# Optimization experiments

Measured on AMD Instinct MI355X. Metric: run time of the kernel, lower is better.

The kernel has to match this reference:

```python
import jax, jax.numpy as jnp
import numpy as np

# static sizes
B, N_PER, D, H, L, DFF, IN_DIM = 32, 1024, 128, 4, 3, 2048, 64
N = B * N_PER
HD = D // H
EPS = 1e-5


def setup_inputs() -> dict:
    key = jax.random.key(0)
    ks = jax.random.split(key, 16)
    s = 0.02
    rn = lambda k, shp: jax.random.normal(k, shp, jnp.float32) * s
    return {
        "x": jax.random.normal(ks[0], (N, IN_DIM), jnp.float32),
        # uniform graph sizes -> static max_nodes; sorted graph ids
        "batch": jnp.repeat(jnp.arange(B, dtype=jnp.int32), N_PER),
        "W_in": rn(ks[1], (D, IN_DIM)),
        "b_in": rn(ks[2], (D,)),
        "Wqkv": rn(ks[3], (L, 3 * D, D)),
        "bqkv": rn(ks[4], (L, 3 * D)),
        "Wo": rn(ks[5], (L, D, D)),
        "bo": rn(ks[6], (L, D)),
        "W1": rn(ks[7], (L, DFF, D)),
        "b1": rn(ks[8], (L, DFF)),
        "W2": rn(ks[9], (L, D, DFF)),
        "b2": rn(ks[10], (L, D)),
        "ln1_g": jnp.ones((L, D), jnp.float32),
        "ln1_b": jnp.zeros((L, D), jnp.float32),
        "ln2_g": jnp.ones((L, D), jnp.float32),
        "ln2_b": jnp.zeros((L, D), jnp.float32),
    }


def _ln(x, g, b):
    m = x.mean(-1, keepdims=True)
    v = jnp.mean((x - m) ** 2, axis=-1, keepdims=True)
    return (x - m) / jnp.sqrt(v + EPS) * g + b


def _mha(h, Wqkv, bqkv, Wo, bo):
    # h: [B, S, D]
    qkv = h @ Wqkv.T + bqkv                      # [B, S, 3D]
    q, k, v = jnp.split(qkv, 3, axis=-1)
    q = q.reshape(B, -1, H, HD)
    k = k.reshape(B, -1, H, HD)
    v = v.reshape(B, -1, H, HD)
    att = jnp.einsum("bqhd,bkhd->bhqk", q, k) / np.sqrt(HD).astype(np.float32)
    p = jax.nn.softmax(att, axis=-1)
    o = jnp.einsum("bhqk,bkhd->bqhd", p, v).reshape(B, -1, D)
    return o @ Wo.T + bo


def reference(x, batch, W_in, b_in, Wqkv, bqkv, Wo, bo, W1, b1, W2, b2,
              ln1_g, ln1_b, ln2_g, ln2_b):
    # fused ragged -> padded: project all nodes once, scatter by (graph, pos)
    h = x @ W_in.T + b_in                        # [N, D]
    starts = jnp.searchsorted(batch, jnp.arange(B, dtype=batch.dtype))
    pos = jnp.arange(N, dtype=batch.dtype) - starts[batch]
    padded = jnp.zeros((B, N_PER, D), h.dtype).at[batch, pos].set(h)

    out = padded
    for l in range(L):  # post-LN TransformerEncoderLayer, dropout=eval
        a = _mha(out, Wqkv[l], bqkv[l], Wo[l], bo[l])
        out = _ln(out + a, ln1_g[l], ln1_b[l])
        f = jax.nn.relu(out @ W1[l].T + b1[l]) @ W2[l].T + b2[l]
        out = _ln(out + f, ln2_g[l], ln2_b[l])

    # mask derived from projected inputs, exactly as the original
    mask = (padded.sum(axis=2) != 0).astype(out.dtype)  # [B, S]
    return (out * mask[:, :, None]).sum(axis=1) / mask.sum(axis=1, keepdims=True)
```

## Files before the change

kernel.cpp:

```cpp
#include <hip/hip_runtime.h>
#include <hip/hip_bf16.h>
#include <stdint.h>

#define BB    32
#define NPER  1024
#define NTOT  32768
#define DD    128
#define HH    4
#define HD    32
#define LL    3
#define DFF   2048
#define INDIM 64
#define QKSCALE 0.17677669529663687f

typedef unsigned short u16;
typedef short bf16x8 __attribute__((ext_vector_type(8)));
typedef float f32x4 __attribute__((ext_vector_type(4)));

#define AS_GLOBAL(p) ((const __attribute__((address_space(1))) void*)(p))
#define AS_LDS(p)    ((__attribute__((address_space(3))) void*)(p))

__device__ __forceinline__ float bf2f(u16 v){
  unsigned u = ((unsigned)v) << 16; float f; __builtin_memcpy(&f, &u, 4); return f;
}
__device__ __forceinline__ u16 f2bf(float f){
  unsigned u; __builtin_memcpy(&u, &f, 4);
  unsigned lsb = (u >> 16) & 1u;
  u += 0x7fffu + lsb;
  return (u16)(u >> 16);
}

constexpr size_t OFF_FLAG   = 0;
constexpr size_t OFF_STARTS = 256;
constexpr size_t OFF_BIN    = 1024;
constexpr size_t OFF_BQKV   = OFF_BIN   + 128*4;
constexpr size_t OFF_BO     = OFF_BQKV  + 1152*4;
constexpr size_t OFF_B1     = OFF_BO    + 384*4;
constexpr size_t OFF_B2     = OFF_B1    + 6144*4;
constexpr size_t OFF_LN1G   = OFF_B2    + 384*4;
constexpr size_t OFF_LN1B   = OFF_LN1G  + 384*4;
constexpr size_t OFF_LN2G   = OFF_LN1B  + 384*4;
constexpr size_t OFF_LN2B   = OFF_LN2G  + 384*4;
constexpr size_t OFF_XB     = 40960;
constexpr size_t OFF_WINB   = OFF_XB    + (size_t)2097152*2;
constexpr size_t OFF_WQKVB  = OFF_WINB  + (size_t)8192*2;
constexpr size_t OFF_WOB    = OFF_WQKVB + (size_t)147456*2;
constexpr size_t OFF_W1B    = OFF_WOB   + (size_t)49152*2;
constexpr size_t OFF_W2B    = OFF_W1B   + (size_t)786432*2;
constexpr size_t OFF_CUR    = OFF_W2B   + (size_t)786432*2;
constexpr size_t OFF_TMP    = OFF_CUR   + (size_t)4194304*4;
constexpr size_t OFF_CURB   = OFF_TMP   + (size_t)4194304*4;
constexpr size_t OFF_QKVB   = OFF_CURB  + (size_t)4194304*2;
constexpr size_t OFF_ATTNOB = OFF_QKVB  + (size_t)12582912*2;
constexpr size_t OFF_ACTB   = OFF_ATTNOB+ (size_t)4194304*2;
constexpr size_t OFF_MASK   = OFF_ACTB  + (size_t)16777216*2;
constexpr size_t OFF_VT     = OFF_MASK  + (size_t)NTOT*4;
constexpr size_t OFF_RED    = OFF_VT    + (size_t)4096*1024*2;
constexpr size_t OFF_CNT    = OFF_RED   + (size_t)32*8*128*4;

__device__ __forceinline__ int plaus(unsigned bits){
  if ((bits << 1) == 0u) return 1;
  unsigned e = (bits >> 23) & 0xFFu;
  return (e >= 100u && e <= 140u) ? 1 : 0;
}
__global__ void detect_kernel(const unsigned* __restrict__ x, int* __restrict__ flag){
  __shared__ int red[256];
  int t = threadIdx.x, c = 0;
  for (int i = t; i < 2048; i += 256){
    unsigned w = x[i];
    c += (plaus(w << 16) & plaus(w & 0xFFFF0000u));
  }
  red[t] = c; __syncthreads();
  for (int s = 128; s > 0; s >>= 1){ if (t < s) red[t] += red[t+s]; __syncthreads(); }
  if (t == 0) *flag = (red[0] >= 1229) ? 1 : 0;
}

__global__ void starts_kernel(const int* __restrict__ batch, int* __restrict__ starts){
  int b = threadIdx.x;
  if (b < BB){
    int lo = 0, hi = NTOT;
    while (lo < hi){ int mid = (lo + hi) >> 1; if (batch[mid] < b) lo = mid + 1; else hi = mid; }
    starts[b] = lo;
  }
}

struct ConvSeg { const void* src; void* dst; int n; int tobf; };
struct ConvArgs { ConvSeg s[15]; };

__global__ __launch_bounds__(256) void convall_kernel(ConvArgs a, const int* __restrict__ flag){
  const int isb = *flag;
  const int blk = blockIdx.x;
  int seg = -1, base = 0, lb = 0;
  #pragma unroll
  for (int i = 0; i < 15; ++i){
    int nb = (a.s[i].n + 1023) >> 10;
    if (seg < 0){
      if (blk < base + nb){ seg = i; lb = blk - base; }
      base += nb;
    }
  }
  const ConvSeg sg = a.s[seg];
  const int idx = lb*1024 + threadIdx.x*4;
  if (idx >= sg.n) return;
  if (sg.tobf){
    u16* dst = (u16*)sg.dst + idx;
    if (isb){
      *(uint2*)dst = *(const uint2*)((const u16*)sg.src + idx);
    } else {
      const float* s4 = (const float*)sg.src + idx;
      dst[0] = f2bf(s4[0]); dst[1] = f2bf(s4[1]);
      dst[2] = f2bf(s4[2]); dst[3] = f2bf(s4[3]);
    }
  } else {
    float* dst = (float*)sg.dst + idx;
    if (isb){
      const u16* s4 = (const u16*)sg.src + idx;
      dst[0] = bf2f(s4[0]); dst[1] = bf2f(s4[1]);
      dst[2] = bf2f(s4[2]); dst[3] = bf2f(s4[3]);
    } else {
      *(float4*)dst = *(const float4*)((const float*)sg.src + idx);
    }
  }
}

__global__ __launch_bounds__(256) void gemm_bf16(
    const u16* __restrict__ A, int lda,
    const u16* __restrict__ W, int ldw,
    const float* __restrict__ bias,
    float* __restrict__ Cf, u16* __restrict__ Cb,
    int N, int K, int flags)
{
  __shared__ __align__(16) u16 At[64][32];
  __shared__ __align__(16) u16 Wt[64][32];
  const int t = threadIdx.x;
  const int m0 = blockIdx.x * 64, n0 = blockIdx.y * 64;
  const int wave = t >> 6, lane = t & 63;
  const int quad = lane >> 4, l16 = lane & 15;
  const int lr = t >> 2, lc = (t & 3) * 8;

  f32x4 acc[4];
  #pragma unroll
  for (int i = 0; i < 4; ++i){ acc[i][0]=0.f; acc[i][1]=0.f; acc[i][2]=0.f; acc[i][3]=0.f; }

  const u16* Arow = A + (size_t)(m0 + lr) * lda + lc;
  const u16* Wrow = W + (size_t)(n0 + lr) * ldw + lc;

  for (int k0 = 0; k0 < K; k0 += 32){
    uint4 av = *(const uint4*)(Arow + k0);
    uint4 wv = *(const uint4*)(Wrow + k0);
    __syncthreads();
    *(uint4*)&At[lr][lc] = av;
    *(uint4*)&Wt[lr][lc] = wv;
    __syncthreads();
    bf16x8 af = *(const bf16x8*)&At[wave*16 + l16][quad*8];
    #pragma unroll
    for (int nt = 0; nt < 4; ++nt){
      bf16x8 wf = *(const bf16x8*)&Wt[nt*16 + l16][quad*8];
      acc[nt] = __builtin_amdgcn_mfma_f32_16x16x32_bf16(af, wf, acc[nt], 0, 0, 0);
    }
  }
  const int row = m0 + wave*16 + quad*4;
  #pragma unroll
  for (int nt = 0; nt < 4; ++nt){
    const int col = n0 + nt*16 + l16;
    const float bv = bias ? bias[col] : 0.f;
    #pragma unroll
    for (int r = 0; r < 4; ++r){
      size_t idx = (size_t)(row + r) * N + col;
      float v = acc[nt][r] + bv;
      if (flags & 1) v = fmaxf(v, 0.f);
      if (Cf) Cf[idx] = v;
      if (Cb) Cb[idx] = f2bf(v);
    }
  }
}

__global__ __launch_bounds__(128) void scatter_kernel(
    const float* __restrict__ hlin, const int* __restrict__ batch,
    const int* __restrict__ starts, float* __restrict__ cur,
    u16* __restrict__ curb, float* __restrict__ mask)
{
  int i = blockIdx.x, t = threadIdx.x;
  int g = batch[i];
  int p = i - starts[g];
  float v = hlin[(size_t)i*DD + t];
  float s = v;
  #pragma unroll
  for (int off = 32; off; off >>= 1) s += __shfl_xor(s, off);
  __shared__ float sh[2];
  if ((t & 63) == 0) sh[t >> 6] = s;
  __syncthreads();
  float rowsum = sh[0] + sh[1];
  if ((unsigned)p < (unsigned)NPER && (unsigned)g < (unsigned)BB){
    size_t j = (size_t)g*NPER + p;
    cur[j*DD + t]  = v;
    curb[j*DD + t] = f2bf(v);
    if (t == 0) mask[j] = (rowsum != 0.f) ? 1.f : 0.f;
  }
}

__global__ __launch_bounds__(256) void fattn_kernel(
    const u16* __restrict__ qkvb,
    const u16* __restrict__ vt,
    u16* __restrict__ attnob)
{
  __shared__ __align__(16) u16 Klds[2][2048];
  __shared__ __align__(16) u16 Vl[2][2048];
  __shared__ __align__(16) u16 Pl[4][16*72];

  const int t = threadIdx.x;
  const int wave = t >> 6, lane = t & 63;
  const int quad = lane >> 4, l16 = lane & 15;
  const int q0 = blockIdx.x * 64;
  const int h = blockIdx.y, b = blockIdx.z;
  const size_t qkvbase = (size_t)b * NPER * 384;
  const u16* Kg = qkvb + qkvbase + 128 + h*HD;
  const u16* Vg = vt + (size_t)((b*HH + h)*HD) * NPER;

  bf16x8 qf;
  {
    const u16* qp = qkvb + qkvbase + (size_t)(q0 + wave*16 + l16)*384 + h*HD + quad*8;
    uint4 qv = *(const uint4*)qp;
    u16 raw[8]; __builtin_memcpy(raw, &qv, 16);
    #pragma unroll
    for (int j = 0; j < 8; ++j) qf[j] = (short)f2bf(bf2f(raw[j]) * QKSCALE);
  }

  const int vcv = wave*2 + (lane >> 5), vd = lane & 31;
  auto stage = [&](int buf, int kt){
    __builtin_amdgcn_global_load_lds(
        AS_GLOBAL(Kg + (size_t)(kt*64 + lane)*384 + wave*8),
        AS_LDS(&Klds[buf][wave*64*8]), 16, 0, 0);
    __builtin_amdgcn_global_load_lds(
        AS_GLOBAL(Vg + (size_t)vd*NPER + kt*64 + vcv*8),
        AS_LDS(&Vl[buf][wave*64*8]), 16, 0, 0);
  };

  float lsum = 0.f;
  f32x4 o0 = {0.f,0.f,0.f,0.f}, o1 = {0.f,0.f,0.f,0.f};
  u16* Pw = &Pl[wave][0];

  stage(0, 0);
  asm volatile("s_waitcnt vmcnt(0)" ::: "memory");
  __syncthreads();

  for (int kt = 0; kt < 16; ++kt){
    const int buf = kt & 1;
    if (kt + 1 < 16) stage(buf ^ 1, kt + 1);

    f32x4 sfr[4];
    #pragma unroll
    for (int nt = 0; nt < 4; ++nt){
      bf16x8 kf = *(const bf16x8*)&Klds[buf][(quad*64 + nt*16 + l16)*8];
      f32x4 z = {0.f,0.f,0.f,0.f};
      sfr[nt] = __builtin_amdgcn_mfma_f32_16x16x32_bf16(kf, qf, z, 0, 0, 0);
    }

    float ps = 0.f;
    #pragma unroll
    for (int nt = 0; nt < 4; ++nt){
      float e0 = __expf(sfr[nt][0]), e1 = __expf(sfr[nt][1]);
      float e2 = __expf(sfr[nt][2]), e3 = __expf(sfr[nt][3]);
      ps += (e0 + e1) + (e2 + e3);
      uint2 w;
      w.x = (unsigned)f2bf(e0) | ((unsigned)f2bf(e1) << 16);
      w.y = (unsigned)f2bf(e2) | ((unsigned)f2bf(e3) << 16);
      *(uint2*)&Pw[l16*72 + nt*16 + quad*4] = w;
    }
    ps += __shfl_xor(ps, 16);
    ps += __shfl_xor(ps, 32);
    lsum += ps;
    asm volatile("s_waitcnt lgkmcnt(0)" ::: "memory");

    #pragma unroll
    for (int kk = 0; kk < 2; ++kk){
      bf16x8 pf = *(const bf16x8*)&Pw[l16*72 + kk*32 + quad*8];
      bf16x8 v0 = *(const bf16x8*)&Vl[buf][((kk*4 + quad)*32 + l16)*8];
      bf16x8 v1 = *(const bf16x8*)&Vl[buf][((kk*4 + quad)*32 + 16 + l16)*8];
      o0 = __builtin_amdgcn_mfma_f32_16x16x32_bf16(pf, v0, o0, 0, 0, 0);
      o1 = __builtin_amdgcn_mfma_f32_16x16x32_bf16(pf, v1, o1, 0, 0, 0);
    }

    if (kt + 1 < 16){
      asm volatile("s_waitcnt vmcnt(0)" ::: "memory");
      __syncthreads();
    }
  }

  #pragma unroll
  for (int r = 0; r < 4; ++r){
    float inv = 1.f / __shfl(lsum, quad*4 + r);
    int row = q0 + wave*16 + quad*4 + r;
    size_t base = (size_t)(b*NPER + row)*DD + h*HD;
    attnob[base + l16]      = f2bf(o0[r] * inv);
    attnob[base + 16 + l16] = f2bf(o1[r] * inv);
  }
}

__device__ __forceinline__ void epilogue_ln64(
    const f32x4 O[8], int m0, int wave, int quad, int l16,
    const float* __restrict__ bias, const float* __restrict__ g,
    const float* __restrict__ beta, float* __restrict__ cur,
    u16* __restrict__ curb)
{
  #pragma unroll
  for (int rr = 0; rr < 4; ++rr){
    int row = m0 + wave*16 + quad*4 + rr;
    float vs[8], sum = 0.f;
    #pragma unroll
    for (int nt = 0; nt < 8; ++nt){
      int col = nt*16 + l16;
      float v = O[nt][rr] + bias[col] + cur[(size_t)row*DD + col];
      vs[nt] = v; sum += v;
    }
    sum += __shfl_xor(sum, 1); sum += __shfl_xor(sum, 2);
    sum += __shfl_xor(sum, 4); sum += __shfl_xor(sum, 8);
    float mean = sum * (1.f/DD);
    float sq = 0.f;
    #pragma unroll
    for (int nt = 0; nt < 8; ++nt){ float d = vs[nt] - mean; sq += d*d; }
    sq += __shfl_xor(sq, 1); sq += __shfl_xor(sq, 2);
    sq += __shfl_xor(sq, 4); sq += __shfl_xor(sq, 8);
    float rs = rsqrtf(sq * (1.f/DD) + 1e-5f);
    #pragma unroll
    for (int nt = 0; nt < 8; ++nt){
      int col = nt*16 + l16;
      float o = (vs[nt] - mean)*rs*g[col] + beta[col];
      cur[(size_t)row*DD + col]  = o;
      curb[(size_t)row*DD + col] = f2bf(o);
    }
  }
}

__global__ __launch_bounds__(256) void wgemm_kernel(
    const u16* __restrict__ A,
    const u16* __restrict__ Wbase,
    const float* __restrict__ biasb,
    int mode,
    u16* __restrict__ outb, int opitch,
    u16* __restrict__ vtout,
    float* __restrict__ cur, u16* __restrict__ curb,
    const float* __restrict__ g, const float* __restrict__ beta)
{
  __shared__ __align__(16) u16 Wl[16384];
  const int t = threadIdx.x, wave = t >> 6, lane = t & 63;
  const int quad = lane >> 4, l16 = lane & 15;
  const int m0 = blockIdx.x * 64, nb = blockIdx.y;
  const u16* Wsl = Wbase + (size_t)nb * 16384;
  const float* bias = biasb + nb * 128;

  #pragma unroll
  for (int j = 0; j < 8; ++j){
    int s = t + 256*j;
    int r = s >> 4, cx = (s & 15) ^ (r & 15);
    *(uint4*)&Wl[s*8] = *(const uint4*)(Wsl + (size_t)r*128 + cx*8);
  }
  bf16x8 af[4];
  #pragma unroll
  for (int kk = 0; kk < 4; ++kk)
    af[kk] = *(const bf16x8*)(A + (size_t)(m0 + wave*16 + l16)*128 + kk*32 + quad*8);
  __syncthreads();

  f32x4 O[8];
  #pragma unroll
  for (int nt = 0; nt < 8; ++nt){ O[nt][0]=0.f; O[nt][1]=0.f; O[nt][2]=0.f; O[nt][3]=0.f; }

  #pragma unroll
  for (int nt = 0; nt < 8; ++nt){
    int row = nt*16 + l16;
    bf16x8 wf[4];
    #pragma unroll
    for (int kk = 0; kk < 4; ++kk)
      wf[kk] = *(const bf16x8*)&Wl[(row*16 + ((kk*4 + quad) ^ l16))*8];
    #pragma unroll
    for (int kk = 0; kk < 4; ++kk)
      O[nt] = __builtin_amdgcn_mfma_f32_16x16x32_bf16(af[kk], wf[kk], O[nt], 0, 0, 0);
  }

  if (mode == 0){
    if (nb == 2 && vtout){
      int rowb = m0 + wave*16 + quad*4;
      int bg = rowb >> 10, s = rowb & 1023;
      #pragma unroll
      for (int nt = 0; nt < 8; ++nt){
        int col = nt*16 + l16;
        int hh = col >> 5, d = col & 31;
        float v0 = O[nt][0] + bias[col], v1 = O[nt][1] + bias[col];
        float v2 = O[nt][2] + bias[col], v3 = O[nt][3] + bias[col];
        uint2 w;
        w.x = (unsigned)f2bf(v0) | ((unsigned)f2bf(v1) << 16);
        w.y = (unsigned)f2bf(v2) | ((unsigned)f2bf(v3) << 16);
        *(uint2*)(vtout + (size_t)((bg*HH + hh)*HD + d)*NPER + s) = w;
      }
    } else {
      #pragma unroll
      for (int rr = 0; rr < 4; ++rr){
        int row = m0 + wave*16 + quad*4 + rr;
        #pragma unroll
        for (int nt = 0; nt < 8; ++nt){
          int col = nt*16 + l16;
          outb[(size_t)row*opitch + nb*128 + col] = f2bf(O[nt][rr] + bias[col]);
        }
      }
    }
  } else {
    epilogue_ln64(O, m0, wave, quad, l16, bias, g, beta, cur, curb);
  }
}

__global__ __launch_bounds__(256, 2) void ffn_kernel(
    const u16* __restrict__ Ag,
    const u16* __restrict__ W1g,
    const u16* __restrict__ W2g,
    const float* __restrict__ b1,
    const float* __restrict__ b2,
    const float* __restrict__ g, const float* __restrict__ beta,
    float* __restrict__ cur, u16* __restrict__ curb)
{
  __shared__ __align__(16) u16 W1l[2][8192];
  __shared__ __align__(16) u16 W2l[2][8192];
  __shared__ __align__(16) u16 Pl[4][16*72];

  const int t = threadIdx.x, wave = t >> 6, lane = t & 63;
  const int quad = lane >> 4, l16 = lane & 15;
  const int m0 = blockIdx.x * 64;
  u16* Pw = &Pl[wave][0];

  auto stage = [&](int buf, int dffc){
    #pragma unroll
    for (int i = 0; i < 4; ++i){
      const int s0 = wave*256 + i*64;
      const int s  = s0 + lane;
      { int r = s >> 4, cx = (s & 15) ^ (r & 15);
        __builtin_amdgcn_global_load_lds(
            AS_GLOBAL(W1g + (size_t)(dffc + r)*128 + cx*8),
            AS_LDS(&W1l[buf][s0*8]), 16, 0, 0); }
      { int r = s >> 3, cx = (s & 7) ^ (r & 7);
        __builtin_amdgcn_global_load_lds(
            AS_GLOBAL(W2g + (size_t)r*DFF + dffc + cx*8),
            AS_LDS(&W2l[buf][s0*8]), 16, 0, 0); }
    }
  };

  bf16x8 af[4];
  #pragma unroll
  for (int kk = 0; kk < 4; ++kk)
    af[kk] = *(const bf16x8*)(Ag + (size_t)(m0 + wave*16 + l16)*128 + kk*32 + quad*8);

  f32x4 O[8];
  #pragma unroll
  for (int nt = 0; nt < 8; ++nt){ O[nt][0]=0.f; O[nt][1]=0.f; O[nt][2]=0.f; O[nt][3]=0.f; }

  stage(0, 0);
  asm volatile("s_waitcnt vmcnt(0)" ::: "memory");
  __syncthreads();

  for (int c = 0; c < 32; ++c){
    const int buf = c & 1;
    if (c + 1 < 32) stage(buf ^ 1, (c + 1)*64);

    #pragma unroll
    for (int nt = 0; nt < 4; ++nt){
      int row = nt*16 + l16;
      bf16x8 wf[4];
      #pragma unroll
      for (int kk = 0; kk < 4; ++kk)
        wf[kk] = *(const bf16x8*)&W1l[buf][(row*16 + ((kk*4 + quad) ^ l16))*8];
      float b1v = b1[c*64 + row];
      f32x4 s = {0.f,0.f,0.f,0.f};
      #pragma unroll
      for (int kk = 0; kk < 4; ++kk)
        s = __builtin_amdgcn_mfma_f32_16x16x32_bf16(af[kk], wf[kk], s, 0, 0, 0);
      #pragma unroll
      for (int rr = 0; rr < 4; ++rr)
        Pw[(quad*4 + rr)*72 + nt*16 + l16] = f2bf(fmaxf(s[rr] + b1v, 0.f));
    }
    asm volatile("s_waitcnt lgkmcnt(0)" ::: "memory");

    bf16x8 pf[2];
    #pragma unroll
    for (int kk = 0; kk < 2; ++kk)
      pf[kk] = *(const bf16x8*)&Pw[l16*72 + kk*32 + quad*8];
    #pragma unroll
    for (int nt = 0; nt < 8; ++nt){
      int row = nt*16 + l16;
      bf16x8 wf[2];
      #pragma unroll
      for (int kk = 0; kk < 2; ++kk)
        wf[kk] = *(const bf16x8*)&W2l[buf][(row*8 + ((kk*4 + quad) ^ (l16 & 7)))*8];
      #pragma unroll
      for (int kk = 0; kk < 2; ++kk)
        O[nt] = __builtin_amdgcn_mfma_f32_16x16x32_bf16(pf[kk], wf[kk], O[nt], 0, 0, 0);
    }

    if (c + 1 < 32){
      asm volatile("s_waitcnt vmcnt(0)" ::: "memory");
      __syncthreads();
    }
  }

  epilogue_ln64(O, m0, wave, quad, l16, b2, g, beta, cur, curb);
}

__global__ __launch_bounds__(128) void reduce1_kernel(
    const float* __restrict__ cur, const float* __restrict__ mask,
    float* __restrict__ partial, float* __restrict__ cnt)
{
  int b = blockIdx.x, c = blockIdx.y, t = threadIdx.x;
  float acc = 0.f, cn = 0.f;
  for (int s = c*128; s < c*128 + 128; ++s){
    float mk = mask[b*NPER + s];
    acc += cur[(size_t)(b*NPER + s)*DD + t] * mk;
    cn += mk;
  }
  partial[(size_t)(b*8 + c)*DD + t] = acc;
  if (t == 0) cnt[b*8 + c] = cn;
}
__global__ __launch_bounds__(128) void reduce2_kernel(
    const float* __restrict__ partial, const float* __restrict__ cnt,
    const int* __restrict__ flag, void* __restrict__ out)
{
  int b = blockIdx.x, t = threadIdx.x;
  float acc = 0.f, cn = 0.f;
  #pragma unroll
  for (int c = 0; c < 8; ++c){
    acc += partial[(size_t)(b*8 + c)*DD + t];
    cn  += cnt[b*8 + c];
  }
  float val = acc / cn;
  if (*flag) ((u16*)out)[b*DD + t] = f2bf(val);
  else       ((float*)out)[b*DD + t] = val;
}

extern "C" void kernel_launch(void* const* d_in, const int* in_sizes, int n_in,
                              void* d_out, int out_size, void* d_ws, size_t ws_size,
                              hipStream_t stream)
{
  (void)in_sizes; (void)n_in; (void)out_size; (void)ws_size;
  char* ws = (char*)d_ws;
  int*   flag   = (int*)(ws + OFF_FLAG);
  int*   starts = (int*)(ws + OFF_STARTS);
  float* BIN  = (float*)(ws + OFF_BIN);
  float* BQKV = (float*)(ws + OFF_BQKV);
  float* BO   = (float*)(ws + OFF_BO);
  float* B1   = (float*)(ws + OFF_B1);
  float* B2   = (float*)(ws + OFF_B2);
  float* LN1G = (float*)(ws + OFF_LN1G);
  float* LN1B = (float*)(ws + OFF_LN1B);
  float* LN2G = (float*)(ws + OFF_LN2G);
  float* LN2B = (float*)(ws + OFF_LN2B);
  u16* XB    = (u16*)(ws + OFF_XB);
  u16* WINB  = (u16*)(ws + OFF_WINB);
  u16* WQKVB = (u16*)(ws + OFF_WQKVB);
  u16* WOB   = (u16*)(ws + OFF_WOB);
  u16* W1B   = (u16*)(ws + OFF_W1B);
  u16* W2B   = (u16*)(ws + OFF_W2B);
  float* CUR = (float*)(ws + OFF_CUR);
  float* TMP = (float*)(ws + OFF_TMP);
  u16* CURB  = (u16*)(ws + OFF_CURB);
  u16* QKVB  = (u16*)(ws + OFF_QKVB);
  u16* ATTNOB= (u16*)(ws + OFF_ATTNOB);
  float* MASK= (float*)(ws + OFF_MASK);
  u16* VT    = (u16*)(ws + OFF_VT);
  float* RED = (float*)(ws + OFF_RED);
  float* CNT = (float*)(ws + OFF_CNT);

  detect_kernel<<<1, 256, 0, stream>>>((const unsigned*)d_in[0], flag);
  starts_kernel<<<1, 64, 0, stream>>>((const int*)d_in[1], starts);

  ConvArgs ca;
  ca.s[0]  = { d_in[0],  XB,    NTOT*INDIM, 1 };
  ca.s[1]  = { d_in[2],  WINB,  DD*INDIM,   1 };
  ca.s[2]  = { d_in[4],  WQKVB, LL*3*DD*DD, 1 };
  ca.s[3]  = { d_in[6],  WOB,   LL*DD*DD,   1 };
  ca.s[4]  = { d_in[8],  W1B,   LL*DFF*DD,  1 };
  ca.s[5]  = { d_in[10], W2B,   LL*DD*DFF,  1 };
  ca.s[6]  = { d_in[3],  BIN,   DD,         0 };
  ca.s[7]  = { d_in[5],  BQKV,  LL*3*DD,    0 };
  ca.s[8]  = { d_in[7],  BO,    LL*DD,      0 };
  ca.s[9]  = { d_in[9],  B1,    LL*DFF,     0 };
  ca.s[10] = { d_in[11], B2,    LL*DD,      0 };
  ca.s[11] = { d_in[12], LN1G,  LL*DD,      0 };
  ca.s[12] = { d_in[13], LN1B,  LL*DD,      0 };
  ca.s[13] = { d_in[14], LN2G,  LL*DD,      0 };
  ca.s[14] = { d_in[15], LN2B,  LL*DD,      0 };
  int nblk = 0;
  for (int i = 0; i < 15; ++i) nblk += (ca.s[i].n + 1023) >> 10;
  convall_kernel<<<nblk, 256, 0, stream>>>(ca, flag);

  gemm_bf16<<<dim3(NTOT/64, DD/64), 256, 0, stream>>>(
      XB, INDIM, WINB, INDIM, BIN, TMP, nullptr, DD, INDIM, 0);
  scatter_kernel<<<NTOT, 128, 0, stream>>>(TMP, (const int*)d_in[1], starts, CUR, CURB, MASK);

  for (int l = 0; l < LL; ++l){
    wgemm_kernel<<<dim3(NTOT/64, 3), 256, 0, stream>>>(
        CURB, WQKVB + (size_t)l*3*DD*DD, BQKV + l*3*DD, 0,
        QKVB, 384, VT, nullptr, nullptr, nullptr, nullptr);
    fattn_kernel<<<dim3(NPER/64, HH, BB), 256, 0, stream>>>(QKVB, VT, ATTNOB);
    wgemm_kernel<<<dim3(NTOT/64, 1), 256, 0, stream>>>(
        ATTNOB, WOB + (size_t)l*DD*DD, BO + l*DD, 1,
        nullptr, 0, nullptr, CUR, CURB, LN1G + l*DD, LN1B + l*DD);
    ffn_kernel<<<dim3(NTOT/64), 256, 0, stream>>>(
        CURB, W1B + (size_t)l*DFF*DD, W2B + (size_t)l*DD*DFF,
        B1 + l*DFF, B2 + l*DD, LN2G + l*DD, LN2B + l*DD, CUR, CURB);
  }

  reduce1_kernel<<<dim3(BB, 8), 128, 0, stream>>>(CUR, MASK, RED, CNT);
  reduce2_kernel<<<BB, 128, 0, stream>>>(RED, CNT, flag, d_out);
}
```

Measured before the change: 508.7 us.

## Process two query tiles per wave in attention and transpose FFN hidden MFMA

The attention kernel now has each wave handle 32 query rows, as two 16-row tiles, instead of 16. This halves the grid and doubles how often each K/V tile staged in LDS is reused, cutting global and LDS staging traffic per query. The FFN first GEMM swaps the MFMA operands so each lane holds four consecutive hidden columns. That allows a vectorized bias load and a single packed 8-byte LDS store instead of four scalar stores. The cost is more registers and LDS per block in attention, and fewer blocks to fill the GPU.

```diff
diff --git a/kernel.cpp b/kernel.cpp
--- a/kernel.cpp
+++ b/kernel.cpp
@@ -206,24 +206,25 @@
 {
   __shared__ __align__(16) u16 Klds[2][2048];
   __shared__ __align__(16) u16 Vl[2][2048];
-  __shared__ __align__(16) u16 Pl[4][16*72];
+  __shared__ __align__(16) u16 Pl[4][2][16*72];
 
   const int t = threadIdx.x;
   const int wave = t >> 6, lane = t & 63;
   const int quad = lane >> 4, l16 = lane & 15;
-  const int q0 = blockIdx.x * 64;
+  const int q0 = blockIdx.x * 128;
   const int h = blockIdx.y, b = blockIdx.z;
   const size_t qkvbase = (size_t)b * NPER * 384;
   const u16* Kg = qkvb + qkvbase + 128 + h*HD;
   const u16* Vg = vt + (size_t)((b*HH + h)*HD) * NPER;
 
-  bf16x8 qf;
-  {
-    const u16* qp = qkvb + qkvbase + (size_t)(q0 + wave*16 + l16)*384 + h*HD + quad*8;
+  bf16x8 qf[2];
+  #pragma unroll
+  for (int qt = 0; qt < 2; ++qt){
+    const u16* qp = qkvb + qkvbase + (size_t)(q0 + wave*32 + qt*16 + l16)*384 + h*HD + quad*8;
     uint4 qv = *(const uint4*)qp;
     u16 raw[8]; __builtin_memcpy(raw, &qv, 16);
     #pragma unroll
-    for (int j = 0; j < 8; ++j) qf[j] = (short)f2bf(bf2f(raw[j]) * QKSCALE);
+    for (int j = 0; j < 8; ++j) qf[qt][j] = (short)f2bf(bf2f(raw[j]) * QKSCALE);
   }
 
   const int vcv = wave*2 + (lane >> 5), vd = lane & 31;
@@ -236,9 +237,12 @@
         AS_LDS(&Vl[buf][wave*64*8]), 16, 0, 0);
   };
 
-  float lsum = 0.f;
-  f32x4 o0 = {0.f,0.f,0.f,0.f}, o1 = {0.f,0.f,0.f,0.f};
-  u16* Pw = &Pl[wave][0];
+  float lsum[2] = {0.f, 0.f};
+  f32x4 o[2][2];
+  #pragma unroll
+  for (int qt = 0; qt < 2; ++qt)
+    #pragma unroll
+    for (int i = 0; i < 2; ++i){ o[qt][i][0]=0.f; o[qt][i][1]=0.f; o[qt][i][2]=0.f; o[qt][i][3]=0.f; }
 
   stage(0, 0);
   asm volatile("s_waitcnt vmcnt(0)" ::: "memory");
@@ -248,37 +252,44 @@
     const int buf = kt & 1;
     if (kt + 1 < 16) stage(buf ^ 1, kt + 1);
 
-    f32x4 sfr[4];
+    f32x4 sfr[2][4];
     #pragma unroll
     for (int nt = 0; nt < 4; ++nt){
       bf16x8 kf = *(const bf16x8*)&Klds[buf][(quad*64 + nt*16 + l16)*8];
       f32x4 z = {0.f,0.f,0.f,0.f};
-      sfr[nt] = __builtin_amdgcn_mfma_f32_16x16x32_bf16(kf, qf, z, 0, 0, 0);
-    }
-
-    float ps = 0.f;
-    #pragma unroll
-    for (int nt = 0; nt < 4; ++nt){
-      float e0 = __expf(sfr[nt][0]), e1 = __expf(sfr[nt][1]);
-      float e2 = __expf(sfr[nt][2]), e3 = __expf(sfr[nt][3]);
-      ps += (e0 + e1) + (e2 + e3);
-      uint2 w;
-      w.x = (unsigned)f2bf(e0) | ((unsigned)f2bf(e1) << 16);
-      w.y = (unsigned)f2bf(e2) | ((unsigned)f2bf(e3) << 16);
-      *(uint2*)&Pw[l16*72 + nt*16 + quad*4] = w;
-    }
-    ps += __shfl_xor(ps, 16);
-    ps += __shfl_xor(ps, 32);
-    lsum += ps;
+      sfr[0][nt] = __builtin_amdgcn_mfma_f32_16x16x32_bf16(kf, qf[0], z, 0, 0, 0);
+      sfr[1][nt] = __builtin_amdgcn_mfma_f32_16x16x32_bf16(kf, qf[1], z, 0, 0, 0);
+    }
+
+    #pragma unroll
+    for (int qt = 0; qt < 2; ++qt){
+      float ps = 0.f;
+      #pragma unroll
+      for (int nt = 0; nt < 4; ++nt){
+        float e0 = __expf(sfr[qt][nt][0]), e1 = __expf(sfr[qt][nt][1]);
+        float e2 = __expf(sfr[qt][nt][2]), e3 = __expf(sfr[qt][nt][3]);
+        ps += (e0 + e1) + (e2 + e3);
+        uint2 w;
+        w.x = (unsigned)f2bf(e0) | ((unsigned)f2bf(e1) << 16);
+        w.y = (unsigned)f2bf(e2) | ((unsigned)f2bf(e3) << 16);
+        *(uint2*)&Pl[wave][qt][l16*72 + nt*16 + quad*4] = w;
+      }
+      ps += __shfl_xor(ps, 16);
+      ps += __shfl_xor(ps, 32);
+      lsum[qt] += ps;
+    }
     asm volatile("s_waitcnt lgkmcnt(0)" ::: "memory");
 
     #pragma unroll
     for (int kk = 0; kk < 2; ++kk){
-      bf16x8 pf = *(const bf16x8*)&Pw[l16*72 + kk*32 + quad*8];
       bf16x8 v0 = *(const bf16x8*)&Vl[buf][((kk*4 + quad)*32 + l16)*8];
       bf16x8 v1 = *(const bf16x8*)&Vl[buf][((kk*4 + quad)*32 + 16 + l16)*8];
-      o0 = __builtin_amdgcn_mfma_f32_16x16x32_bf16(pf, v0, o0, 0, 0, 0);
-      o1 = __builtin_amdgcn_mfma_f32_16x16x32_bf16(pf, v1, o1, 0, 0, 0);
+      #pragma unroll
+      for (int qt = 0; qt < 2; ++qt){
+        bf16x8 pf = *(const bf16x8*)&Pl[wave][qt][l16*72 + kk*32 + quad*8];
+        o[qt][0] = __builtin_amdgcn_mfma_f32_16x16x32_bf16(pf, v0, o[qt][0], 0, 0, 0);
+        o[qt][1] = __builtin_amdgcn_mfma_f32_16x16x32_bf16(pf, v1, o[qt][1], 0, 0, 0);
+      }
     }
 
     if (kt + 1 < 16){
@@ -288,12 +299,15 @@
   }
 
   #pragma unroll
-  for (int r = 0; r < 4; ++r){
-    float inv = 1.f / __shfl(lsum, quad*4 + r);
-    int row = q0 + wave*16 + quad*4 + r;
-    size_t base = (size_t)(b*NPER + row)*DD + h*HD;
-    attnob[base + l16]      = f2bf(o0[r] * inv);
-    attnob[base + 16 + l16] = f2bf(o1[r] * inv);
+  for (int qt = 0; qt < 2; ++qt){
+    #pragma unroll
+    for (int r = 0; r < 4; ++r){
+      float inv = 1.f / __shfl(lsum[qt], quad*4 + r);
+      int row = q0 + wave*32 + qt*16 + quad*4 + r;
+      size_t base = (size_t)(b*NPER + row)*DD + h*HD;
+      attnob[base + l16]      = f2bf(o[qt][0][r] * inv);
+      attnob[base + 16 + l16] = f2bf(o[qt][1][r] * inv);
+    }
   }
 }
 
@@ -466,14 +480,17 @@
       #pragma unroll
       for (int kk = 0; kk < 4; ++kk)
         wf[kk] = *(const bf16x8*)&W1l[buf][(row*16 + ((kk*4 + quad) ^ l16))*8];
-      float b1v = b1[c*64 + row];
+      f32x4 b1v = *(const f32x4*)&b1[c*64 + nt*16 + quad*4];
       f32x4 s = {0.f,0.f,0.f,0.f};
       #pragma unroll
       for (int kk = 0; kk < 4; ++kk)
-        s = __builtin_amdgcn_mfma_f32_16x16x32_bf16(af[kk], wf[kk], s, 0, 0, 0);
-      #pragma unroll
-      for (int rr = 0; rr < 4; ++rr)
-        Pw[(quad*4 + rr)*72 + nt*16 + l16] = f2bf(fmaxf(s[rr] + b1v, 0.f));
+        s = __builtin_amdgcn_mfma_f32_16x16x32_bf16(wf[kk], af[kk], s, 0, 0, 0);
+      float v0 = fmaxf(s[0] + b1v[0], 0.f), v1 = fmaxf(s[1] + b1v[1], 0.f);
+      float v2 = fmaxf(s[2] + b1v[2], 0.f), v3 = fmaxf(s[3] + b1v[3], 0.f);
+      uint2 w;
+      w.x = (unsigned)f2bf(v0) | ((unsigned)f2bf(v1) << 16);
+      w.y = (unsigned)f2bf(v2) | ((unsigned)f2bf(v3) << 16);
+      *(uint2*)&Pw[l16*72 + nt*16 + quad*4] = w;
     }
     asm volatile("s_waitcnt lgkmcnt(0)" ::: "memory");
 
@@ -596,7 +613,7 @@
     wgemm_kernel<<<dim3(NTOT/64, 3), 256, 0, stream>>>(
         CURB, WQKVB + (size_t)l*3*DD*DD, BQKV + l*3*DD, 0,
         QKVB, 384, VT, nullptr, nullptr, nullptr, nullptr);
-    fattn_kernel<<<dim3(NPER/64, HH, BB), 256, 0, stream>>>(QKVB, VT, ATTNOB);
+    fattn_kernel<<<dim3(NPER/128, HH, BB), 256, 0, stream>>>(QKVB, VT, ATTNOB);
     wgemm_kernel<<<dim3(NTOT/64, 1), 256, 0, stream>>>(
         ATTNOB, WOB + (size_t)l*DD*DD, BO + l*DD, 1,
         nullptr, 0, nullptr, CUR, CURB, LN1G + l*DD, LN1B + l*DD);
```

Measured after the change: 507.8 us. About the same (-0.2%).
